# Optimization experiments

Measured on AMD Instinct MI355X. Metric: run time of the kernel, lower is better.

Reference implementation:

```python
import jax, jax.numpy as jnp
import numpy as np

T, L, N, DR = 8, 8, 500, 32
D = 2 * DR          # dr2 = 64
K = 12              # neighbors per region
S = 2               # number_sp attention layers


def setup_inputs() -> dict:
    key = jax.random.key(0)
    ks = jax.random.split(key, 14)
    inp = {}
    inp["all_data_static"] = jax.random.normal(ks[0], (T, L, N, D), jnp.float32)
    inp["thre_nc"] = jax.random.uniform(ks[1], (T, L, N, 1), jnp.float32)
    inp["all_data_dynamic_now"] = jax.random.uniform(ks[2], (L, N, D), jnp.float32)
    inp["neigh_poi"] = jax.random.randint(ks[3], (N, K), 0, N)
    inp["neigh_road"] = jax.random.randint(ks[4], (N, K), 0, N)
    inp["neigh_record"] = jax.random.randint(ks[5], (N, K), 0, N)
    inp["w1"] = jax.random.normal(ks[6], (2 * D, D), jnp.float32) * 0.05
    inp["wq_all"] = jax.random.normal(ks[7], (2, 3, S, D, D), jnp.float32) * 0.05
    inp["wk_all"] = jax.random.normal(ks[8], (2, 3, S, D, D), jnp.float32) * 0.05
    inp["wd_all"] = jax.random.normal(ks[9], (2, 3, S, D, D), jnp.float32) * 0.05
    inp["wmix_all"] = jax.random.normal(ks[10], (2, 3, D), jnp.float32) * 0.1
    inp["conv_w"] = jax.random.normal(ks[11], (4, 2 * D + 1), jnp.float32) * 0.05
    inp["conv_b"] = jnp.zeros((4,), jnp.float32)
    inp["fin_w"] = jax.random.normal(ks[12], (N, N), jnp.float32) * 0.02
    inp["fin_b"] = jnp.ones((N,), jnp.float32)
    return inp


def _attention(data, neigh, wq, wk, wd):
    # data: (T,L,N,D), neigh: (N,K)
    dn = data[:, :, neigh, :]                                   # (T,L,N,K,D) gather
    q = jnp.einsum('tlnd,de->tlne', data, wq)                   # (T,L,N,D)
    k = jnp.einsum('tlnkd,de->tlnke', dn, wk)                   # (T,L,N,K,D)
    a = jax.nn.softmax(jnp.einsum('tlne,tlnke->tlnk', q, k), -1)
    out = q + jnp.einsum('tlnk,tlnke->tlne', a, k)              # residual on q
    return jax.nn.sigmoid(jnp.einsum('tlnd,de->tlne', out, wd))


def _multiattention(data, neighs, wq, wk, wd, wmix):
    outs = []
    for g in range(3):  # poi, road, record
        x = data
        for s in range(wq.shape[1]):
            x = _attention(x, neighs[g], wq[g, s], wk[g, s], wd[g, s])
        outs.append(x)
    return jax.nn.sigmoid(outs[0] * wmix[0] + outs[1] * wmix[1] + outs[2] * wmix[2])


def reference(all_data_static, thre_nc, all_data_dynamic_now,
              neigh_poi, neigh_road, neigh_record,
              w1, wq_all, wk_all, wd_all, wmix_all,
              conv_w, conv_b, fin_w, fin_b):
    # --- Evolution: gated recurrence over time steps 1..T-1 ---
    def evo_step(now, xs):
        st, th = xs  # (L,N,D), (L,N,1)
        new = jax.nn.sigmoid(jnp.concatenate([now, st], -1) @ w1 * th
                             + now * (1.0 - th))
        return new, (new, new - now)
    now_final, (dyn_rest, diffs) = jax.lax.scan(
        evo_step, all_data_dynamic_now, (all_data_static[1:], thre_nc[1:]))
    all_dyn = jnp.concatenate([all_data_dynamic_now[None], dyn_rest], 0)  # (T,L,N,D)

    neighs = (neigh_poi, neigh_road, neigh_record)
    dyn = _multiattention(all_dyn, neighs, wq_all[0], wk_all[0], wd_all[0], wmix_all[0])
    sta = _multiattention(all_data_static, neighs, wq_all[1], wk_all[1], wd_all[1], wmix_all[1])
    x = jnp.concatenate([dyn, sta], -1)                          # (T,L,N,2D)

    # --- ConvLSTM, kernel (1,1), hidden_dim=1 -> pointwise gated recurrence ---
    h0 = jnp.zeros((x.shape[0], x.shape[2], 1), x.dtype)         # (T,N,1)
    def cell(carry, xt):  # xt: (T,N,2D)
        h, c = carry
        gates = jnp.concatenate([xt, h], -1) @ conv_w.T + conv_b  # (T,N,4)
        i = jax.nn.sigmoid(gates[..., 0:1])
        f = jax.nn.sigmoid(gates[..., 1:2])
        o = jax.nn.sigmoid(gates[..., 2:3])
        g = jnp.tanh(gates[..., 3:4])
        c2 = f * c + i * g
        h2 = o * jnp.tanh(c2)
        return (h2, c2), None
    (h_last, _), _ = jax.lax.scan(cell, (h0, h0), jnp.swapaxes(x, 0, 1))

    out = jax.nn.sigmoid(h_last[..., 0] @ fin_w.T + fin_b)       # (T,N)
    return out, now_final, diffs
```

## Files before the change

kernel.cpp:

```cpp
#include <hip/hip_runtime.h>
#include <math.h>

namespace {
constexpr int kT = 8, kL = 8, kN = 500, kD = 64, kK = 12;
constexpr int kLN  = kL * kN;
constexpr int kTLN = kT * kL * kN;
constexpr int kBUF = kTLN * kD;
constexpr int XS = 68;
}

__device__ __forceinline__ float sigf(float v) { return 1.f / (1.f + __expf(-v)); }

__device__ __forceinline__ void stage_x(const float* __restrict__ src, float* lds,
                                        int row0, int M) {
    int r  = threadIdx.x >> 4;
    int c4 = (threadIdx.x & 15) << 2;
#pragma unroll
    for (int i = 0; i < 4; ++i) {
        int rr  = r + 16 * i;
        int row = row0 + rr;
        row = row < M ? row : M - 1;
        float4 v = *reinterpret_cast<const float4*>(src + (size_t)row * 64 + c4);
        *reinterpret_cast<float4*>(lds + rr * XS + c4) = v;
    }
}

template <int K>
__device__ __forceinline__ void stage_w(const float* __restrict__ w, float* lds) {
    const float4* s = reinterpret_cast<const float4*>(w);
    float4* d = reinterpret_cast<float4*>(lds);
#pragma unroll
    for (int i = 0; i < K / 16; ++i)
        d[threadIdx.x + 256 * i] = s[threadIdx.x + 256 * i];
}

__device__ __forceinline__ void gemm_core(const float* ldsx, const float* ldsw,
                                          int rblk, int cblk, float4 acc[4]) {
#pragma unroll 4
    for (int k = 0; k < 64; k += 4) {
        float4 xv[4], wv[4];
#pragma unroll
        for (int i = 0; i < 4; ++i)
            xv[i] = *reinterpret_cast<const float4*>(ldsx + (4 * rblk + i) * XS + k);
#pragma unroll
        for (int d = 0; d < 4; ++d)
            wv[d] = *reinterpret_cast<const float4*>(ldsw + (k + d) * 64 + 4 * cblk);
#pragma unroll
        for (int i = 0; i < 4; ++i) {
            float xs[4] = {xv[i].x, xv[i].y, xv[i].z, xv[i].w};
#pragma unroll
            for (int d = 0; d < 4; ++d) {
                acc[i].x = fmaf(xs[d], wv[d].x, acc[i].x);
                acc[i].y = fmaf(xs[d], wv[d].y, acc[i].y);
                acc[i].z = fmaf(xs[d], wv[d].z, acc[i].z);
                acc[i].w = fmaf(xs[d], wv[d].w, acc[i].w);
            }
        }
    }
}

__device__ __forceinline__ void gemm_core_gw(const float* ldsx,
                                             const float* __restrict__ gw,
                                             int rblk, int cblk, float4 acc[4]) {
#pragma unroll 4
    for (int k = 0; k < 64; k += 4) {
        float4 xv[4], wv[4];
#pragma unroll
        for (int i = 0; i < 4; ++i)
            xv[i] = *reinterpret_cast<const float4*>(ldsx + (4 * rblk + i) * XS + k);
#pragma unroll
        for (int d = 0; d < 4; ++d)
            wv[d] = *reinterpret_cast<const float4*>(gw + (k + d) * 64 + 4 * cblk);
#pragma unroll
        for (int i = 0; i < 4; ++i) {
            float xs[4] = {xv[i].x, xv[i].y, xv[i].z, xv[i].w};
#pragma unroll
            for (int d = 0; d < 4; ++d) {
                acc[i].x = fmaf(xs[d], wv[d].x, acc[i].x);
                acc[i].y = fmaf(xs[d], wv[d].y, acc[i].y);
                acc[i].z = fmaf(xs[d], wv[d].z, acc[i].z);
                acc[i].w = fmaf(xs[d], wv[d].w, acc[i].w);
            }
        }
    }
}

__device__ __forceinline__ void gemm_core2(const float* ldsx, const float* ldswa,
                                           const float* ldswb, int rblk, int cblk,
                                           float4 acca[4], float4 accb[4]) {
#pragma unroll 4
    for (int k = 0; k < 64; k += 4) {
        float4 xv[4], wa[4], wb[4];
#pragma unroll
        for (int i = 0; i < 4; ++i)
            xv[i] = *reinterpret_cast<const float4*>(ldsx + (4 * rblk + i) * XS + k);
#pragma unroll
        for (int d = 0; d < 4; ++d) {
            wa[d] = *reinterpret_cast<const float4*>(ldswa + (k + d) * 64 + 4 * cblk);
            wb[d] = *reinterpret_cast<const float4*>(ldswb + (k + d) * 64 + 4 * cblk);
        }
#pragma unroll
        for (int i = 0; i < 4; ++i) {
            float xs[4] = {xv[i].x, xv[i].y, xv[i].z, xv[i].w};
#pragma unroll
            for (int d = 0; d < 4; ++d) {
                acca[i].x = fmaf(xs[d], wa[d].x, acca[i].x);
                acca[i].y = fmaf(xs[d], wa[d].y, acca[i].y);
                acca[i].z = fmaf(xs[d], wa[d].z, acca[i].z);
                acca[i].w = fmaf(xs[d], wa[d].w, acca[i].w);
                accb[i].x = fmaf(xs[d], wb[d].x, accb[i].x);
                accb[i].y = fmaf(xs[d], wb[d].y, accb[i].y);
                accb[i].z = fmaf(xs[d], wb[d].z, accb[i].z);
                accb[i].w = fmaf(xs[d], wb[d].w, accb[i].w);
            }
        }
    }
}

__global__ void __launch_bounds__(256) evo_all_kernel(const float* __restrict__ stat,
                                                      const float* __restrict__ thre,
                                                      const float* __restrict__ dyn0,
                                                      float* __restrict__ all_dyn,
                                                      float* __restrict__ diff,
                                                      float* __restrict__ now_final,
                                                      const float* __restrict__ w1) {
    __shared__ float ldsn[64 * XS];
    __shared__ float ldss[64 * XS];
    __shared__ float ldsw[128 * 64];
    int row0 = blockIdx.x * 64;
    stage_x(dyn0, ldsn, row0, kLN);
    stage_w<128>(w1, ldsw);
    int rblk = threadIdx.x >> 4, cblk = threadIdx.x & 15;
    __syncthreads();
#pragma unroll
    for (int i = 0; i < 4; ++i) {
        int row = row0 + 4 * rblk + i;
        if (row < kLN) {
            float4 x0 = *reinterpret_cast<const float4*>(ldsn + (4 * rblk + i) * XS + 4 * cblk);
            *reinterpret_cast<float4*>(all_dyn + (size_t)row * 64 + 4 * cblk) = x0;
        }
    }
#pragma unroll 1
    for (int t = 1; t < kT; ++t) {
        stage_x(stat + (size_t)t * kLN * kD, ldss, row0, kLN);
        __syncthreads();
        float4 acc[4] = {};
        gemm_core(ldsn, ldsw, rblk, cblk, acc);
        gemm_core(ldss, ldsw + 64 * 64, rblk, cblk, acc);
        float4 nv[4];
#pragma unroll
        for (int i = 0; i < 4; ++i) {
            int row = row0 + 4 * rblk + i;
            int rc  = row < kLN ? row : kLN - 1;
            float tt = thre[t * kLN + rc];
            float4 xn = *reinterpret_cast<const float4*>(ldsn + (4 * rblk + i) * XS + 4 * cblk);
            nv[i].x = sigf(acc[i].x * tt + xn.x * (1.f - tt));
            nv[i].y = sigf(acc[i].y * tt + xn.y * (1.f - tt));
            nv[i].z = sigf(acc[i].z * tt + xn.z * (1.f - tt));
            nv[i].w = sigf(acc[i].w * tt + xn.w * (1.f - tt));
            if (row < kLN) {
                float4 df;
                df.x = nv[i].x - xn.x; df.y = nv[i].y - xn.y;
                df.z = nv[i].z - xn.z; df.w = nv[i].w - xn.w;
                *reinterpret_cast<float4*>(all_dyn + ((size_t)t * kLN + row) * 64 + 4 * cblk) = nv[i];
                *reinterpret_cast<float4*>(diff + ((size_t)(t - 1) * kLN + row) * 64 + 4 * cblk) = df;
                if (t == kT - 1)
                    *reinterpret_cast<float4*>(now_final + (size_t)row * 64 + 4 * cblk) = nv[i];
            }
        }
        __syncthreads();
#pragma unroll
        for (int i = 0; i < 4; ++i)
            *reinterpret_cast<float4*>(ldsn + (4 * rblk + i) * XS + 4 * cblk) = nv[i];
    }
}

__global__ void __launch_bounds__(256) gemm_qk(const float* __restrict__ Xdyn,
                                               const float* __restrict__ Xstat,
                                               const float* __restrict__ wq_all,
                                               const float* __restrict__ wk_all,
                                               float* __restrict__ b1,
                                               float* __restrict__ b2, int step) {
    __shared__ float ldsx[64 * XS];
    __shared__ float ldswq[64 * 64];
    __shared__ float ldswk[64 * 64];
    int c = blockIdx.y;
    int m = c / 3;
    float* b1c = b1 + (size_t)c * kBUF;
    float* b2c = b2 + (size_t)c * kBUF;
    const float* X = step ? b1c : (m == 0 ? Xdyn : Xstat);
    size_t woff = (size_t)(c * 2 + step) * kD * kD;
    int row0 = blockIdx.x * 64;
    stage_x(X, ldsx, row0, kTLN);
    stage_w<64>(wq_all + woff, ldswq);
    stage_w<64>(wk_all + woff, ldswk);
    __syncthreads();
    int rblk = threadIdx.x >> 4, cblk = threadIdx.x & 15;
    float4 aq[4] = {}, ak[4] = {};
    gemm_core2(ldsx, ldswq, ldswk, rblk, cblk, aq, ak);
#pragma unroll
    for (int i = 0; i < 4; ++i) {
        size_t row = row0 + 4 * rblk + i;
        *reinterpret_cast<float4*>(b1c + row * 64 + 4 * cblk) = aq[i];
        *reinterpret_cast<float4*>(b2c + row * 64 + 4 * cblk) = ak[i];
    }
}

__global__ void __launch_bounds__(256) scorewd_kernel(float* __restrict__ b1,
                                                      const float* __restrict__ b2,
                                                      const int* __restrict__ npoi,
                                                      const int* __restrict__ nroad,
                                                      const int* __restrict__ nrec,
                                                      const float* __restrict__ wd_all,
                                                      int step) {
    __shared__ float ldsx[64 * XS];
    int p   = blockIdx.y * gridDim.x + blockIdx.x;
    int xcd = p & 7;
    int gid = xcd * 375 + (p >> 3);
    int c    = gid / 500;
    int tile = gid - c * 500;
    int g = c % 3;
    float* b1c = b1 + (size_t)c * kBUF;
    const float* b2c = b2 + (size_t)c * kBUF;
    const int* neigh = (g == 0) ? npoi : (g == 1) ? nroad : nrec;
    const float* gw = wd_all + (size_t)(c * 2 + step) * kD * kD;

    int lane = threadIdx.x & 63;
    int wv   = threadIdx.x >> 6;
    int sub  = lane >> 4;
    int gq   = lane & 15;
    int row0 = tile * 64;
#pragma unroll 1
    for (int pp = 0; pp < 4; ++pp) {
        int lr  = pp * 16 + wv * 4 + sub;
        int row = row0 + lr;
        int n   = row % kN;
        int slab = row - n;
        float4 q = *(reinterpret_cast<const float4*>(b1c) + (size_t)row * 16 + gq);
        const int4* nbp = reinterpret_cast<const int4*>(neigh + n * kK);
        int4 nb0 = nbp[0], nb1 = nbp[1], nb2 = nbp[2];
        int nb[12] = {nb0.x, nb0.y, nb0.z, nb0.w, nb1.x, nb1.y, nb1.z, nb1.w,
                      nb2.x, nb2.y, nb2.z, nb2.w};
        float4 kv[12];
        float sc[12];
#pragma unroll
        for (int j = 0; j < 12; ++j) {
            kv[j] = *(reinterpret_cast<const float4*>(b2c) + (size_t)(slab + nb[j]) * 16 + gq);
            sc[j] = q.x * kv[j].x + q.y * kv[j].y + q.z * kv[j].z + q.w * kv[j].w;
        }
#pragma unroll
        for (int off = 1; off < 16; off <<= 1) {
#pragma unroll
            for (int j = 0; j < 12; ++j) sc[j] += __shfl_xor(sc[j], off, 16);
        }
        float mx = sc[0];
#pragma unroll
        for (int j = 1; j < 12; ++j) mx = fmaxf(mx, sc[j]);
        float ssum = 0.f;
#pragma unroll
        for (int j = 0; j < 12; ++j) { sc[j] = __expf(sc[j] - mx); ssum += sc[j]; }
        float inv = 1.f / ssum;
        float4 o = q;
#pragma unroll
        for (int j = 0; j < 12; ++j) {
            float a = sc[j] * inv;
            o.x = fmaf(a, kv[j].x, o.x);
            o.y = fmaf(a, kv[j].y, o.y);
            o.z = fmaf(a, kv[j].z, o.z);
            o.w = fmaf(a, kv[j].w, o.w);
        }
        *reinterpret_cast<float4*>(ldsx + lr * XS + 4 * gq) = o;
    }
    __syncthreads();
    int rblk = threadIdx.x >> 4, cblk = threadIdx.x & 15;
    float4 acc[4] = {};
    gemm_core_gw(ldsx, gw, rblk, cblk, acc);
#pragma unroll
    for (int i = 0; i < 4; ++i) {
        size_t idx = ((size_t)(row0 + 4 * rblk + i)) * 64 + 4 * cblk;
        float4 y;
        y.x = sigf(acc[i].x); y.y = sigf(acc[i].y);
        y.z = sigf(acc[i].z); y.w = sigf(acc[i].w);
        *reinterpret_cast<float4*>(b1c + idx) = y;
    }
}

__global__ void __launch_bounds__(256) lstm_kernel(const float* __restrict__ b1,
                                                   const float* __restrict__ wmix,
                                                   const float* __restrict__ cw,
                                                   const float* __restrict__ cb,
                                                   float* __restrict__ hlast) {
    int lane = threadIdx.x & 63;
    int wv   = threadIdx.x >> 6;
    int sub  = lane >> 4;
    int fq   = lane & 15;
    int cell = blockIdx.x * 16 + wv * 4 + sub;
    int t = cell / kN, n = cell % kN;
    float wd_[4][4], ws_[4][4], wh[4], bb[4];
#pragma unroll
    for (int gg = 0; gg < 4; ++gg) {
#pragma unroll
        for (int k = 0; k < 4; ++k) {
            wd_[gg][k] = cw[gg * 129 + fq * 4 + k];
            ws_[gg][k] = cw[gg * 129 + 64 + fq * 4 + k];
        }
        wh[gg] = cw[gg * 129 + 128];
        bb[gg] = cb[gg];
    }
    float4 wm[6];
#pragma unroll
    for (int j = 0; j < 6; ++j)
        wm[j] = *reinterpret_cast<const float4*>(wmix + j * 64 + fq * 4);
    float h = 0.f, cc = 0.f;
#pragma unroll 1
    for (int l = 0; l < kL; ++l) {
        size_t row16 = ((size_t)(t * kL + l) * kN + n) * 16 + fq;
        float4 y[6];
#pragma unroll
        for (int j = 0; j < 6; ++j)
            y[j] = *(reinterpret_cast<const float4*>(b1) + (size_t)j * (kBUF / 4) + row16);
        float4 xd, xs;
        xd.x = sigf(y[0].x * wm[0].x + y[1].x * wm[1].x + y[2].x * wm[2].x);
        xd.y = sigf(y[0].y * wm[0].y + y[1].y * wm[1].y + y[2].y * wm[2].y);
        xd.z = sigf(y[0].z * wm[0].z + y[1].z * wm[1].z + y[2].z * wm[2].z);
        xd.w = sigf(y[0].w * wm[0].w + y[1].w * wm[1].w + y[2].w * wm[2].w);
        xs.x = sigf(y[3].x * wm[3].x + y[4].x * wm[4].x + y[5].x * wm[5].x);
        xs.y = sigf(y[3].y * wm[3].y + y[4].y * wm[4].y + y[5].y * wm[5].y);
        xs.z = sigf(y[3].z * wm[3].z + y[4].z * wm[4].z + y[5].z * wm[5].z);
        xs.w = sigf(y[3].w * wm[3].w + y[4].w * wm[4].w + y[5].w * wm[5].w);
        float gsum[4];
#pragma unroll
        for (int gg = 0; gg < 4; ++gg) {
            float v = xd.x * wd_[gg][0] + xd.y * wd_[gg][1]
                    + xd.z * wd_[gg][2] + xd.w * wd_[gg][3];
            v += xs.x * ws_[gg][0] + xs.y * ws_[gg][1]
               + xs.z * ws_[gg][2] + xs.w * ws_[gg][3];
            gsum[gg] = v;
        }
#pragma unroll
        for (int off = 1; off < 16; off <<= 1) {
#pragma unroll
            for (int gg = 0; gg < 4; ++gg) gsum[gg] += __shfl_xor(gsum[gg], off, 16);
        }
        float gi = sigf(gsum[0] + bb[0] + h * wh[0]);
        float gf = sigf(gsum[1] + bb[1] + h * wh[1]);
        float go = sigf(gsum[2] + bb[2] + h * wh[2]);
        float gg_ = tanhf(gsum[3] + bb[3] + h * wh[3]);
        cc = gf * cc + gi * gg_;
        h = go * tanhf(cc);
    }
    if (fq == 0) hlast[cell] = h;
}

__global__ void final_kernel(const float* __restrict__ h, const float* __restrict__ fw,
                             const float* __restrict__ fb, float* __restrict__ out) {
    int wave = threadIdx.x >> 6, lane = threadIdx.x & 63;
    int o = blockIdx.x * 4 + wave;
    int t = o / kN, m = o % kN;
    float acc = 0.f;
    for (int n = lane; n < kN; n += 64)
        acc = fmaf(h[t * kN + n], fw[(size_t)m * kN + n], acc);
#pragma unroll
    for (int off = 32; off > 0; off >>= 1) acc += __shfl_xor(acc, off);
    if (lane == 0) out[o] = sigf(acc + fb[m]);
}

extern "C" void kernel_launch(void* const* d_in, const int* in_sizes, int n_in,
                              void* d_out, int out_size, void* d_ws, size_t ws_size,
                              hipStream_t stream) {
    const float* stat   = (const float*)d_in[0];
    const float* thre   = (const float*)d_in[1];
    const float* dyn0   = (const float*)d_in[2];
    const int*   npoi   = (const int*)d_in[3];
    const int*   nroad  = (const int*)d_in[4];
    const int*   nrec   = (const int*)d_in[5];
    const float* w1     = (const float*)d_in[6];
    const float* wq_all = (const float*)d_in[7];
    const float* wk_all = (const float*)d_in[8];
    const float* wd_all = (const float*)d_in[9];
    const float* wmix   = (const float*)d_in[10];
    const float* conv_w = (const float*)d_in[11];
    const float* conv_b = (const float*)d_in[12];
    const float* fin_w  = (const float*)d_in[13];
    const float* fin_b  = (const float*)d_in[14];

    float* out       = (float*)d_out;
    float* now_final = out + kT * kN;
    float* diffs     = now_final + (size_t)kLN * kD;

    float* ws      = (float*)d_ws;
    float* all_dyn = ws;
    float* b1      = ws + (size_t)kBUF;
    float* b2      = ws + 7 * (size_t)kBUF;
    float* hlast   = ws + 13 * (size_t)kBUF;

    evo_all_kernel<<<(kLN + 63) / 64, 256, 0, stream>>>(stat, thre, dyn0,
                                                        all_dyn, diffs, now_final, w1);

    dim3 agrid(kTLN / 64, 6);
    gemm_qk<<<agrid, 256, 0, stream>>>(all_dyn, stat, wq_all, wk_all, b1, b2, 0);
    scorewd_kernel<<<agrid, 256, 0, stream>>>(b1, b2, npoi, nroad, nrec, wd_all, 0);
    gemm_qk<<<agrid, 256, 0, stream>>>(all_dyn, stat, wq_all, wk_all, b1, b2, 1);
    scorewd_kernel<<<agrid, 256, 0, stream>>>(b1, b2, npoi, nroad, nrec, wd_all, 1);

    lstm_kernel<<<kT * kN / 16, 256, 0, stream>>>(b1, wmix, conv_w, conv_b, hlast);
    final_kernel<<<kT * kN / 4, 256, 0, stream>>>(hlast, fin_w, fin_b, out);
}
```

Measured before the change: 350.7 us.

## Fuse score/Wd with next-layer QK GEMM and store K in bf16

Merges the first attention layer's score+Wd stage with the second layer's Q/K projection into one kernel, so the intermediate activation never goes back to global memory and one launch disappears. K is now stored as bf16 to halve the traffic of the neighbor gathers. Weights are read straight from global/cache instead of being staged in LDS. The fusion needs a separate K buffer, because another block's layer-1 K gather could otherwise race with layer-2 K writes. bf16 K adds rounding error to the attention scores and outputs.

Measured after the change: 384.9 us. 1.1x slower.

```diff
diff --git a/kernel.cpp b/kernel.cpp
--- a/kernel.cpp
+++ b/kernel.cpp
@@ -11,6 +11,18 @@
 
 __device__ __forceinline__ float sigf(float v) { return 1.f / (1.f + __expf(-v)); }
 
+__device__ __forceinline__ uint2 pack_bf16x4(float4 v) {
+    auto r = [](float f) {
+        unsigned u = __float_as_uint(f);
+        u += 0x7FFFu + ((u >> 16) & 1u);
+        return u >> 16;
+    };
+    uint2 o;
+    o.x = r(v.x) | (r(v.y) << 16);
+    o.y = r(v.z) | (r(v.w) << 16);
+    return o;
+}
+
 __device__ __forceinline__ void stage_x(const float* __restrict__ src, float* lds,
                                         int row0, int M) {
     int r  = threadIdx.x >> 4;
@@ -85,9 +97,11 @@
     }
 }
 
-__device__ __forceinline__ void gemm_core2(const float* ldsx, const float* ldswa,
-                                           const float* ldswb, int rblk, int cblk,
-                                           float4 acca[4], float4 accb[4]) {
+__device__ __forceinline__ void gemm_core2_gw(const float* ldsx,
+                                              const float* __restrict__ gwa,
+                                              const float* __restrict__ gwb,
+                                              int rblk, int cblk,
+                                              float4 acca[4], float4 accb[4]) {
 #pragma unroll 4
     for (int k = 0; k < 64; k += 4) {
         float4 xv[4], wa[4], wb[4];
@@ -96,8 +110,8 @@
             xv[i] = *reinterpret_cast<const float4*>(ldsx + (4 * rblk + i) * XS + k);
 #pragma unroll
         for (int d = 0; d < 4; ++d) {
-            wa[d] = *reinterpret_cast<const float4*>(ldswa + (k + d) * 64 + 4 * cblk);
-            wb[d] = *reinterpret_cast<const float4*>(ldswb + (k + d) * 64 + 4 * cblk);
+            wa[d] = *reinterpret_cast<const float4*>(gwa + (k + d) * 64 + 4 * cblk);
+            wb[d] = *reinterpret_cast<const float4*>(gwb + (k + d) * 64 + 4 * cblk);
         }
 #pragma unroll
         for (int i = 0; i < 4; ++i) {
@@ -114,6 +128,67 @@
                 accb[i].w = fmaf(xs[d], wb[d].w, accb[i].w);
             }
         }
+    }
+}
+
+__device__ __forceinline__ void score_phase(const float* __restrict__ Qsrc,
+                                            const uint2* __restrict__ Kb,
+                                            const int* __restrict__ neigh,
+                                            float* ldsx, int row0) {
+    int lane = threadIdx.x & 63;
+    int wv   = threadIdx.x >> 6;
+    int sub  = lane >> 4;
+    int gq   = lane & 15;
+    float4 qv[4];
+#pragma unroll
+    for (int pp = 0; pp < 4; ++pp) {
+        int row = row0 + pp * 16 + wv * 4 + sub;
+        qv[pp] = *(reinterpret_cast<const float4*>(Qsrc) + (size_t)row * 16 + gq);
+    }
+#pragma unroll 1
+    for (int pp = 0; pp < 4; ++pp) {
+        int lr  = pp * 16 + wv * 4 + sub;
+        int row = row0 + lr;
+        int n   = row % kN;
+        int slab = row - n;
+        float4 q = qv[pp];
+        const int4* nbp = reinterpret_cast<const int4*>(neigh + n * kK);
+        int4 nb0 = nbp[0], nb1 = nbp[1], nb2 = nbp[2];
+        int nb[12] = {nb0.x, nb0.y, nb0.z, nb0.w, nb1.x, nb1.y, nb1.z, nb1.w,
+                      nb2.x, nb2.y, nb2.z, nb2.w};
+        float4 kv[12];
+        float sc[12];
+#pragma unroll
+        for (int j = 0; j < 12; ++j) {
+            uint2 kk = Kb[(size_t)(slab + nb[j]) * 16 + gq];
+            kv[j].x = __uint_as_float(kk.x << 16);
+            kv[j].y = __uint_as_float(kk.x & 0xFFFF0000u);
+            kv[j].z = __uint_as_float(kk.y << 16);
+            kv[j].w = __uint_as_float(kk.y & 0xFFFF0000u);
+            sc[j] = q.x * kv[j].x + q.y * kv[j].y + q.z * kv[j].z + q.w * kv[j].w;
+        }
+#pragma unroll
+        for (int off = 1; off < 16; off <<= 1) {
+#pragma unroll
+            for (int j = 0; j < 12; ++j) sc[j] += __shfl_xor(sc[j], off, 16);
+        }
+        float mx = sc[0];
+#pragma unroll
+        for (int j = 1; j < 12; ++j) mx = fmaxf(mx, sc[j]);
+        float ssum = 0.f;
+#pragma unroll
+        for (int j = 0; j < 12; ++j) { sc[j] = __expf(sc[j] - mx); ssum += sc[j]; }
+        float inv = 1.f / ssum;
+        float4 o = q;
+#pragma unroll
+        for (int j = 0; j < 12; ++j) {
+            float a = sc[j] * inv;
+            o.x = fmaf(a, kv[j].x, o.x);
+            o.y = fmaf(a, kv[j].y, o.y);
+            o.z = fmaf(a, kv[j].z, o.z);
+            o.w = fmaf(a, kv[j].w, o.w);
+        }
+        *reinterpret_cast<float4*>(ldsx + lr * XS + 4 * gq) = o;
     }
 }
 
@@ -175,44 +250,43 @@
     }
 }
 
-__global__ void __launch_bounds__(256) gemm_qk(const float* __restrict__ Xdyn,
-                                               const float* __restrict__ Xstat,
-                                               const float* __restrict__ wq_all,
-                                               const float* __restrict__ wk_all,
-                                               float* __restrict__ b1,
-                                               float* __restrict__ b2, int step) {
+__global__ void __launch_bounds__(256) gemm_qk0(const float* __restrict__ Xdyn,
+                                                const float* __restrict__ Xstat,
+                                                const float* __restrict__ wq_all,
+                                                const float* __restrict__ wk_all,
+                                                float* __restrict__ b1,
+                                                unsigned short* __restrict__ b2a) {
     __shared__ float ldsx[64 * XS];
-    __shared__ float ldswq[64 * 64];
-    __shared__ float ldswk[64 * 64];
     int c = blockIdx.y;
     int m = c / 3;
+    const float* X = (m == 0) ? Xdyn : Xstat;
+    const float* gwq = wq_all + (size_t)(c * 2) * kD * kD;
+    const float* gwk = wk_all + (size_t)(c * 2) * kD * kD;
     float* b1c = b1 + (size_t)c * kBUF;
-    float* b2c = b2 + (size_t)c * kBUF;
-    const float* X = step ? b1c : (m == 0 ? Xdyn : Xstat);
-    size_t woff = (size_t)(c * 2 + step) * kD * kD;
+    unsigned short* kc = b2a + (size_t)c * kBUF;
     int row0 = blockIdx.x * 64;
     stage_x(X, ldsx, row0, kTLN);
-    stage_w<64>(wq_all + woff, ldswq);
-    stage_w<64>(wk_all + woff, ldswk);
     __syncthreads();
     int rblk = threadIdx.x >> 4, cblk = threadIdx.x & 15;
     float4 aq[4] = {}, ak[4] = {};
-    gemm_core2(ldsx, ldswq, ldswk, rblk, cblk, aq, ak);
+    gemm_core2_gw(ldsx, gwq, gwk, rblk, cblk, aq, ak);
 #pragma unroll
     for (int i = 0; i < 4; ++i) {
         size_t row = row0 + 4 * rblk + i;
         *reinterpret_cast<float4*>(b1c + row * 64 + 4 * cblk) = aq[i];
-        *reinterpret_cast<float4*>(b2c + row * 64 + 4 * cblk) = ak[i];
-    }
-}
-
-__global__ void __launch_bounds__(256) scorewd_kernel(float* __restrict__ b1,
-                                                      const float* __restrict__ b2,
-                                                      const int* __restrict__ npoi,
-                                                      const int* __restrict__ nroad,
-                                                      const int* __restrict__ nrec,
-                                                      const float* __restrict__ wd_all,
-                                                      int step) {
+        *reinterpret_cast<uint2*>(kc + row * 64 + 4 * cblk) = pack_bf16x4(ak[i]);
+    }
+}
+
+__global__ void __launch_bounds__(256) swqk_kernel(float* __restrict__ b1,
+                                                   const unsigned short* __restrict__ b2a,
+                                                   unsigned short* __restrict__ b2b,
+                                                   const int* __restrict__ npoi,
+                                                   const int* __restrict__ nroad,
+                                                   const int* __restrict__ nrec,
+                                                   const float* __restrict__ wd_all,
+                                                   const float* __restrict__ wq_all,
+                                                   const float* __restrict__ wk_all) {
     __shared__ float ldsx[64 * XS];
     int p   = blockIdx.y * gridDim.x + blockIdx.x;
     int xcd = p & 7;
@@ -221,60 +295,64 @@
     int tile = gid - c * 500;
     int g = c % 3;
     float* b1c = b1 + (size_t)c * kBUF;
-    const float* b2c = b2 + (size_t)c * kBUF;
+    const uint2* Kb = reinterpret_cast<const uint2*>(b2a + (size_t)c * kBUF);
+    unsigned short* k1c = b2b + (size_t)c * kBUF;
     const int* neigh = (g == 0) ? npoi : (g == 1) ? nroad : nrec;
-    const float* gw = wd_all + (size_t)(c * 2 + step) * kD * kD;
-
-    int lane = threadIdx.x & 63;
-    int wv   = threadIdx.x >> 6;
-    int sub  = lane >> 4;
-    int gq   = lane & 15;
+    const float* gwd = wd_all + (size_t)(c * 2) * kD * kD;
+    const float* gwq = wq_all + (size_t)(c * 2 + 1) * kD * kD;
+    const float* gwk = wk_all + (size_t)(c * 2 + 1) * kD * kD;
     int row0 = tile * 64;
-#pragma unroll 1
-    for (int pp = 0; pp < 4; ++pp) {
-        int lr  = pp * 16 + wv * 4 + sub;
-        int row = row0 + lr;
-        int n   = row % kN;
-        int slab = row - n;
-        float4 q = *(reinterpret_cast<const float4*>(b1c) + (size_t)row * 16 + gq);
-        const int4* nbp = reinterpret_cast<const int4*>(neigh + n * kK);
-        int4 nb0 = nbp[0], nb1 = nbp[1], nb2 = nbp[2];
-        int nb[12] = {nb0.x, nb0.y, nb0.z, nb0.w, nb1.x, nb1.y, nb1.z, nb1.w,
-                      nb2.x, nb2.y, nb2.z, nb2.w};
-        float4 kv[12];
-        float sc[12];
-#pragma unroll
-        for (int j = 0; j < 12; ++j) {
-            kv[j] = *(reinterpret_cast<const float4*>(b2c) + (size_t)(slab + nb[j]) * 16 + gq);
-            sc[j] = q.x * kv[j].x + q.y * kv[j].y + q.z * kv[j].z + q.w * kv[j].w;
-        }
-#pragma unroll
-        for (int off = 1; off < 16; off <<= 1) {
-#pragma unroll
-            for (int j = 0; j < 12; ++j) sc[j] += __shfl_xor(sc[j], off, 16);
-        }
-        float mx = sc[0];
-#pragma unroll
-        for (int j = 1; j < 12; ++j) mx = fmaxf(mx, sc[j]);
-        float ssum = 0.f;
-#pragma unroll
-        for (int j = 0; j < 12; ++j) { sc[j] = __expf(sc[j] - mx); ssum += sc[j]; }
-        float inv = 1.f / ssum;
-        float4 o = q;
-#pragma unroll
-        for (int j = 0; j < 12; ++j) {
-            float a = sc[j] * inv;
-            o.x = fmaf(a, kv[j].x, o.x);
-            o.y = fmaf(a, kv[j].y, o.y);
-            o.z = fmaf(a, kv[j].z, o.z);
-            o.w = fmaf(a, kv[j].w, o.w);
-        }
-        *reinterpret_cast<float4*>(ldsx + lr * XS + 4 * gq) = o;
-    }
-    __syncthreads();
+
+    score_phase(b1c, Kb, neigh, ldsx, row0);
+    __syncthreads();
+
     int rblk = threadIdx.x >> 4, cblk = threadIdx.x & 15;
     float4 acc[4] = {};
-    gemm_core_gw(ldsx, gw, rblk, cblk, acc);
+    gemm_core_gw(ldsx, gwd, rblk, cblk, acc);
+    __syncthreads();
+#pragma unroll
+    for (int i = 0; i < 4; ++i) {
+        float4 y;
+        y.x = sigf(acc[i].x); y.y = sigf(acc[i].y);
+        y.z = sigf(acc[i].z); y.w = sigf(acc[i].w);
+        *reinterpret_cast<float4*>(ldsx + (4 * rblk + i) * XS + 4 * cblk) = y;
+    }
+    __syncthreads();
+    float4 aq[4] = {}, ak[4] = {};
+    gemm_core2_gw(ldsx, gwq, gwk, rblk, cblk, aq, ak);
+#pragma unroll
+    for (int i = 0; i < 4; ++i) {
+        size_t row = row0 + 4 * rblk + i;
+        *reinterpret_cast<float4*>(b1c + row * 64 + 4 * cblk) = aq[i];
+        *reinterpret_cast<uint2*>(k1c + row * 64 + 4 * cblk) = pack_bf16x4(ak[i]);
+    }
+}
+
+__global__ void __launch_bounds__(256) scorewd_kernel(float* __restrict__ b1,
+                                                      const unsigned short* __restrict__ b2b,
+                                                      const int* __restrict__ npoi,
+                                                      const int* __restrict__ nroad,
+                                                      const int* __restrict__ nrec,
+                                                      const float* __restrict__ wd_all) {
+    __shared__ float ldsx[64 * XS];
+    int p   = blockIdx.y * gridDim.x + blockIdx.x;
+    int xcd = p & 7;
+    int gid = xcd * 375 + (p >> 3);
+    int c    = gid / 500;
+    int tile = gid - c * 500;
+    int g = c % 3;
+    float* b1c = b1 + (size_t)c * kBUF;
+    const uint2* Kb = reinterpret_cast<const uint2*>(b2b + (size_t)c * kBUF);
+    const int* neigh = (g == 0) ? npoi : (g == 1) ? nroad : nrec;
+    const float* gwd = wd_all + (size_t)(c * 2 + 1) * kD * kD;
+    int row0 = tile * 64;
+
+    score_phase(b1c, Kb, neigh, ldsx, row0);
+    __syncthreads();
+
+    int rblk = threadIdx.x >> 4, cblk = threadIdx.x & 15;
+    float4 acc[4] = {};
+    gemm_core_gw(ldsx, gwd, rblk, cblk, acc);
 #pragma unroll
     for (int i = 0; i < 4; ++i) {
         size_t idx = ((size_t)(row0 + 4 * rblk + i)) * 64 + 4 * cblk;
@@ -391,17 +469,18 @@
     float* ws      = (float*)d_ws;
     float* all_dyn = ws;
     float* b1      = ws + (size_t)kBUF;
-    float* b2      = ws + 7 * (size_t)kBUF;
+    unsigned short* b2a = (unsigned short*)(ws + 7 * (size_t)kBUF);
+    unsigned short* b2b = (unsigned short*)(ws + 10 * (size_t)kBUF);
     float* hlast   = ws + 13 * (size_t)kBUF;
 
     evo_all_kernel<<<(kLN + 63) / 64, 256, 0, stream>>>(stat, thre, dyn0,
                                                         all_dyn, diffs, now_final, w1);
 
     dim3 agrid(kTLN / 64, 6);
-    gemm_qk<<<agrid, 256, 0, stream>>>(all_dyn, stat, wq_all, wk_all, b1, b2, 0);
-    scorewd_kernel<<<agrid, 256, 0, stream>>>(b1, b2, npoi, nroad, nrec, wd_all, 0);
-    gemm_qk<<<agrid, 256, 0, stream>>>(all_dyn, stat, wq_all, wk_all, b1, b2, 1);
-    scorewd_kernel<<<agrid, 256, 0, stream>>>(b1, b2, npoi, nroad, nrec, wd_all, 1);
+    gemm_qk0<<<agrid, 256, 0, stream>>>(all_dyn, stat, wq_all, wk_all, b1, b2a);
+    swqk_kernel<<<agrid, 256, 0, stream>>>(b1, b2a, b2b, npoi, nroad, nrec,
+                                           wd_all, wq_all, wk_all);
+    scorewd_kernel<<<agrid, 256, 0, stream>>>(b1, b2b, npoi, nroad, nrec, wd_all);
 
     lstm_kernel<<<kT * kN / 16, 256, 0, stream>>>(b1, wmix, conv_w, conv_b, hlast);
     final_kernel<<<kT * kN / 4, 256, 0, stream>>>(hlast, fin_w, fin_b, out);
```

## Store attention keys as bf16, halve row tiles, read weights from global

Applied to the files above, without the earlier changes.

The key projection buffer is now written as bf16 (round-to-nearest-even packing) and unpacked in the score kernel. This halves the gather traffic for the 12-neighbor key reads. Tiles shrink from 64 to 32 rows per block, doubling the grid for the recurrence and attention kernels. gemm_qk now reads Wq/Wk directly from global memory instead of staging them in LDS. Reduced key precision may change results slightly, and smaller tiles reuse each weight load over fewer rows.

Measured after the change: 460.7 us. 1.31x slower.

```diff
diff --git a/kernel.cpp b/kernel.cpp
--- a/kernel.cpp
+++ b/kernel.cpp
@@ -11,16 +11,26 @@
 
 __device__ __forceinline__ float sigf(float v) { return 1.f / (1.f + __expf(-v)); }
 
-__device__ __forceinline__ void stage_x(const float* __restrict__ src, float* lds,
-                                        int row0, int M) {
+__device__ __forceinline__ uint2 pack_bf16x4(float4 v) {
+    auto r = [](float f) {
+        unsigned u = __float_as_uint(f);
+        u += 0x7FFFu + ((u >> 16) & 1u);
+        return u >> 16;
+    };
+    uint2 o;
+    o.x = r(v.x) | (r(v.y) << 16);
+    o.y = r(v.z) | (r(v.w) << 16);
+    return o;
+}
+
+__device__ __forceinline__ void stage_x32(const float* __restrict__ src, float* lds,
+                                          int row0) {
     int r  = threadIdx.x >> 4;
     int c4 = (threadIdx.x & 15) << 2;
 #pragma unroll
-    for (int i = 0; i < 4; ++i) {
-        int rr  = r + 16 * i;
-        int row = row0 + rr;
-        row = row < M ? row : M - 1;
-        float4 v = *reinterpret_cast<const float4*>(src + (size_t)row * 64 + c4);
+    for (int i = 0; i < 2; ++i) {
+        int rr = r + 16 * i;
+        float4 v = *reinterpret_cast<const float4*>(src + (size_t)(row0 + rr) * 64 + c4);
         *reinterpret_cast<float4*>(lds + rr * XS + c4) = v;
     }
 }
@@ -34,19 +44,19 @@
         d[threadIdx.x + 256 * i] = s[threadIdx.x + 256 * i];
 }
 
-__device__ __forceinline__ void gemm_core(const float* ldsx, const float* ldsw,
-                                          int rblk, int cblk, float4 acc[4]) {
+__device__ __forceinline__ void gemm_core32(const float* ldsx, const float* w,
+                                            int rblk, int cblk, float4 acc[2]) {
 #pragma unroll 4
     for (int k = 0; k < 64; k += 4) {
-        float4 xv[4], wv[4];
-#pragma unroll
-        for (int i = 0; i < 4; ++i)
-            xv[i] = *reinterpret_cast<const float4*>(ldsx + (4 * rblk + i) * XS + k);
+        float4 xv[2], wv[4];
+#pragma unroll
+        for (int i = 0; i < 2; ++i)
+            xv[i] = *reinterpret_cast<const float4*>(ldsx + (2 * rblk + i) * XS + k);
 #pragma unroll
         for (int d = 0; d < 4; ++d)
-            wv[d] = *reinterpret_cast<const float4*>(ldsw + (k + d) * 64 + 4 * cblk);
-#pragma unroll
-        for (int i = 0; i < 4; ++i) {
+            wv[d] = *reinterpret_cast<const float4*>(w + (k + d) * 64 + 4 * cblk);
+#pragma unroll
+        for (int i = 0; i < 2; ++i) {
             float xs[4] = {xv[i].x, xv[i].y, xv[i].z, xv[i].w};
 #pragma unroll
             for (int d = 0; d < 4; ++d) {
@@ -59,61 +69,90 @@
     }
 }
 
-__device__ __forceinline__ void gemm_core_gw(const float* ldsx,
-                                             const float* __restrict__ gw,
-                                             int rblk, int cblk, float4 acc[4]) {
+__device__ __forceinline__ void gemm_core32x2(const float* ldsx, const float* wa,
+                                              const float* wb, int rblk, int cblk,
+                                              float4 acca[2], float4 accb[2]) {
 #pragma unroll 4
     for (int k = 0; k < 64; k += 4) {
-        float4 xv[4], wv[4];
-#pragma unroll
-        for (int i = 0; i < 4; ++i)
-            xv[i] = *reinterpret_cast<const float4*>(ldsx + (4 * rblk + i) * XS + k);
-#pragma unroll
-        for (int d = 0; d < 4; ++d)
-            wv[d] = *reinterpret_cast<const float4*>(gw + (k + d) * 64 + 4 * cblk);
-#pragma unroll
-        for (int i = 0; i < 4; ++i) {
+        float4 xv[2], va[4], vb[4];
+#pragma unroll
+        for (int i = 0; i < 2; ++i)
+            xv[i] = *reinterpret_cast<const float4*>(ldsx + (2 * rblk + i) * XS + k);
+#pragma unroll
+        for (int d = 0; d < 4; ++d) {
+            va[d] = *reinterpret_cast<const float4*>(wa + (k + d) * 64 + 4 * cblk);
+            vb[d] = *reinterpret_cast<const float4*>(wb + (k + d) * 64 + 4 * cblk);
+        }
+#pragma unroll
+        for (int i = 0; i < 2; ++i) {
             float xs[4] = {xv[i].x, xv[i].y, xv[i].z, xv[i].w};
 #pragma unroll
             for (int d = 0; d < 4; ++d) {
-                acc[i].x = fmaf(xs[d], wv[d].x, acc[i].x);
-                acc[i].y = fmaf(xs[d], wv[d].y, acc[i].y);
-                acc[i].z = fmaf(xs[d], wv[d].z, acc[i].z);
-                acc[i].w = fmaf(xs[d], wv[d].w, acc[i].w);
+                acca[i].x = fmaf(xs[d], va[d].x, acca[i].x);
+                acca[i].y = fmaf(xs[d], va[d].y, acca[i].y);
+                acca[i].z = fmaf(xs[d], va[d].z, acca[i].z);
+                acca[i].w = fmaf(xs[d], va[d].w, acca[i].w);
+                accb[i].x = fmaf(xs[d], vb[d].x, accb[i].x);
+                accb[i].y = fmaf(xs[d], vb[d].y, accb[i].y);
+                accb[i].z = fmaf(xs[d], vb[d].z, accb[i].z);
+                accb[i].w = fmaf(xs[d], vb[d].w, accb[i].w);
             }
         }
     }
 }
 
-__device__ __forceinline__ void gemm_core2(const float* ldsx, const float* ldswa,
-                                           const float* ldswb, int rblk, int cblk,
-                                           float4 acca[4], float4 accb[4]) {
-#pragma unroll 4
-    for (int k = 0; k < 64; k += 4) {
-        float4 xv[4], wa[4], wb[4];
-#pragma unroll
-        for (int i = 0; i < 4; ++i)
-            xv[i] = *reinterpret_cast<const float4*>(ldsx + (4 * rblk + i) * XS + k);
-#pragma unroll
-        for (int d = 0; d < 4; ++d) {
-            wa[d] = *reinterpret_cast<const float4*>(ldswa + (k + d) * 64 + 4 * cblk);
-            wb[d] = *reinterpret_cast<const float4*>(ldswb + (k + d) * 64 + 4 * cblk);
-        }
-#pragma unroll
-        for (int i = 0; i < 4; ++i) {
-            float xs[4] = {xv[i].x, xv[i].y, xv[i].z, xv[i].w};
-#pragma unroll
-            for (int d = 0; d < 4; ++d) {
-                acca[i].x = fmaf(xs[d], wa[d].x, acca[i].x);
-                acca[i].y = fmaf(xs[d], wa[d].y, acca[i].y);
-                acca[i].z = fmaf(xs[d], wa[d].z, acca[i].z);
-                acca[i].w = fmaf(xs[d], wa[d].w, acca[i].w);
-                accb[i].x = fmaf(xs[d], wb[d].x, accb[i].x);
-                accb[i].y = fmaf(xs[d], wb[d].y, accb[i].y);
-                accb[i].z = fmaf(xs[d], wb[d].z, accb[i].z);
-                accb[i].w = fmaf(xs[d], wb[d].w, accb[i].w);
-            }
-        }
+__device__ __forceinline__ void score_phase32(const float* __restrict__ Qsrc,
+                                              const uint2* __restrict__ Kb,
+                                              const int* __restrict__ neigh,
+                                              float* ldsx, int row0) {
+    int lane = threadIdx.x & 63;
+    int wv   = threadIdx.x >> 6;
+    int sub  = lane >> 4;
+    int gq   = lane & 15;
+#pragma unroll 1
+    for (int pp = 0; pp < 2; ++pp) {
+        int lr  = pp * 16 + wv * 4 + sub;
+        int row = row0 + lr;
+        int n   = row % kN;
+        int slab = row - n;
+        float4 q = *(reinterpret_cast<const float4*>(Qsrc) + (size_t)row * 16 + gq);
+        const int4* nbp = reinterpret_cast<const int4*>(neigh + n * kK);
+        int4 nb0 = nbp[0], nb1 = nbp[1], nb2 = nbp[2];
+        int nb[12] = {nb0.x, nb0.y, nb0.z, nb0.w, nb1.x, nb1.y, nb1.z, nb1.w,
+                      nb2.x, nb2.y, nb2.z, nb2.w};
+        float4 kv[12];
+        float sc[12];
+#pragma unroll
+        for (int j = 0; j < 12; ++j) {
+            uint2 kk = Kb[(size_t)(slab + nb[j]) * 16 + gq];
+            kv[j].x = __uint_as_float(kk.x << 16);
+            kv[j].y = __uint_as_float(kk.x & 0xFFFF0000u);
+            kv[j].z = __uint_as_float(kk.y << 16);
+            kv[j].w = __uint_as_float(kk.y & 0xFFFF0000u);
+            sc[j] = q.x * kv[j].x + q.y * kv[j].y + q.z * kv[j].z + q.w * kv[j].w;
+        }
+#pragma unroll
+        for (int off = 1; off < 16; off <<= 1) {
+#pragma unroll
+            for (int j = 0; j < 12; ++j) sc[j] += __shfl_xor(sc[j], off, 16);
+        }
+        float mx = sc[0];
+#pragma unroll
+        for (int j = 1; j < 12; ++j) mx = fmaxf(mx, sc[j]);
+        float ssum = 0.f;
+#pragma unroll
+        for (int j = 0; j < 12; ++j) { sc[j] = __expf(sc[j] - mx); ssum += sc[j]; }
+        float inv = 1.f / ssum;
+        float4 o = q;
+#pragma unroll
+        for (int j = 0; j < 12; ++j) {
+            float a = sc[j] * inv;
+            o.x = fmaf(a, kv[j].x, o.x);
+            o.y = fmaf(a, kv[j].y, o.y);
+            o.z = fmaf(a, kv[j].z, o.z);
+            o.w = fmaf(a, kv[j].w, o.w);
+        }
+        *reinterpret_cast<float4*>(ldsx + lr * XS + 4 * gq) = o;
     }
 }
 
@@ -124,54 +163,49 @@
                                                       float* __restrict__ diff,
                                                       float* __restrict__ now_final,
                                                       const float* __restrict__ w1) {
-    __shared__ float ldsn[64 * XS];
-    __shared__ float ldss[64 * XS];
+    __shared__ float ldsn[32 * XS];
+    __shared__ float ldss[32 * XS];
     __shared__ float ldsw[128 * 64];
-    int row0 = blockIdx.x * 64;
-    stage_x(dyn0, ldsn, row0, kLN);
+    int row0 = blockIdx.x * 32;
+    stage_x32(dyn0, ldsn, row0);
     stage_w<128>(w1, ldsw);
     int rblk = threadIdx.x >> 4, cblk = threadIdx.x & 15;
     __syncthreads();
 #pragma unroll
-    for (int i = 0; i < 4; ++i) {
-        int row = row0 + 4 * rblk + i;
-        if (row < kLN) {
-            float4 x0 = *reinterpret_cast<const float4*>(ldsn + (4 * rblk + i) * XS + 4 * cblk);
-            *reinterpret_cast<float4*>(all_dyn + (size_t)row * 64 + 4 * cblk) = x0;
-        }
+    for (int i = 0; i < 2; ++i) {
+        int row = row0 + 2 * rblk + i;
+        float4 x0 = *reinterpret_cast<const float4*>(ldsn + (2 * rblk + i) * XS + 4 * cblk);
+        *reinterpret_cast<float4*>(all_dyn + (size_t)row * 64 + 4 * cblk) = x0;
     }
 #pragma unroll 1
     for (int t = 1; t < kT; ++t) {
-        stage_x(stat + (size_t)t * kLN * kD, ldss, row0, kLN);
+        stage_x32(stat + (size_t)t * kLN * kD, ldss, row0);
         __syncthreads();
-        float4 acc[4] = {};
-        gemm_core(ldsn, ldsw, rblk, cblk, acc);
-        gemm_core(ldss, ldsw + 64 * 64, rblk, cblk, acc);
-        float4 nv[4];
-#pragma unroll
-        for (int i = 0; i < 4; ++i) {
-            int row = row0 + 4 * rblk + i;
-            int rc  = row < kLN ? row : kLN - 1;
-            float tt = thre[t * kLN + rc];
-            float4 xn = *reinterpret_cast<const float4*>(ldsn + (4 * rblk + i) * XS + 4 * cblk);
+        float4 acc[2] = {};
+        gemm_core32(ldsn, ldsw, rblk, cblk, acc);
+        gemm_core32(ldss, ldsw + 64 * 64, rblk, cblk, acc);
+        float4 nv[2];
+#pragma unroll
+        for (int i = 0; i < 2; ++i) {
+            int row = row0 + 2 * rblk + i;
+            float tt = thre[t * kLN + row];
+            float4 xn = *reinterpret_cast<const float4*>(ldsn + (2 * rblk + i) * XS + 4 * cblk);
             nv[i].x = sigf(acc[i].x * tt + xn.x * (1.f - tt));
             nv[i].y = sigf(acc[i].y * tt + xn.y * (1.f - tt));
             nv[i].z = sigf(acc[i].z * tt + xn.z * (1.f - tt));
             nv[i].w = sigf(acc[i].w * tt + xn.w * (1.f - tt));
-            if (row < kLN) {
-                float4 df;
-                df.x = nv[i].x - xn.x; df.y = nv[i].y - xn.y;
-                df.z = nv[i].z - xn.z; df.w = nv[i].w - xn.w;
-                *reinterpret_cast<float4*>(all_dyn + ((size_t)t * kLN + row) * 64 + 4 * cblk) = nv[i];
-                *reinterpret_cast<float4*>(diff + ((size_t)(t - 1) * kLN + row) * 64 + 4 * cblk) = df;
-                if (t == kT - 1)
-                    *reinterpret_cast<float4*>(now_final + (size_t)row * 64 + 4 * cblk) = nv[i];
-            }
+            float4 df;
+            df.x = nv[i].x - xn.x; df.y = nv[i].y - xn.y;
+            df.z = nv[i].z - xn.z; df.w = nv[i].w - xn.w;
+            *reinterpret_cast<float4*>(all_dyn + ((size_t)t * kLN + row) * 64 + 4 * cblk) = nv[i];
+            *reinterpret_cast<float4*>(diff + ((size_t)(t - 1) * kLN + row) * 64 + 4 * cblk) = df;
+            if (t == kT - 1)
+                *reinterpret_cast<float4*>(now_final + (size_t)row * 64 + 4 * cblk) = nv[i];
         }
         __syncthreads();
 #pragma unroll
-        for (int i = 0; i < 4; ++i)
-            *reinterpret_cast<float4*>(ldsn + (4 * rblk + i) * XS + 4 * cblk) = nv[i];
+        for (int i = 0; i < 2; ++i)
+            *reinterpret_cast<float4*>(ldsn + (2 * rblk + i) * XS + 4 * cblk) = nv[i];
     }
 }
 
@@ -180,104 +214,59 @@
                                                const float* __restrict__ wq_all,
                                                const float* __restrict__ wk_all,
                                                float* __restrict__ b1,
-                                               float* __restrict__ b2, int step) {
-    __shared__ float ldsx[64 * XS];
-    __shared__ float ldswq[64 * 64];
-    __shared__ float ldswk[64 * 64];
+                                               unsigned short* __restrict__ b2,
+                                               int step) {
+    __shared__ float ldsx[32 * XS];
     int c = blockIdx.y;
     int m = c / 3;
     float* b1c = b1 + (size_t)c * kBUF;
-    float* b2c = b2 + (size_t)c * kBUF;
+    unsigned short* kc = b2 + (size_t)c * kBUF;
     const float* X = step ? b1c : (m == 0 ? Xdyn : Xstat);
-    size_t woff = (size_t)(c * 2 + step) * kD * kD;
-    int row0 = blockIdx.x * 64;
-    stage_x(X, ldsx, row0, kTLN);
-    stage_w<64>(wq_all + woff, ldswq);
-    stage_w<64>(wk_all + woff, ldswk);
+    const float* gwq = wq_all + (size_t)(c * 2 + step) * kD * kD;
+    const float* gwk = wk_all + (size_t)(c * 2 + step) * kD * kD;
+    int row0 = blockIdx.x * 32;
+    stage_x32(X, ldsx, row0);
     __syncthreads();
     int rblk = threadIdx.x >> 4, cblk = threadIdx.x & 15;
-    float4 aq[4] = {}, ak[4] = {};
-    gemm_core2(ldsx, ldswq, ldswk, rblk, cblk, aq, ak);
-#pragma unroll
-    for (int i = 0; i < 4; ++i) {
-        size_t row = row0 + 4 * rblk + i;
+    float4 aq[2] = {}, ak[2] = {};
+    gemm_core32x2(ldsx, gwq, gwk, rblk, cblk, aq, ak);
+#pragma unroll
+    for (int i = 0; i < 2; ++i) {
+        size_t row = row0 + 2 * rblk + i;
         *reinterpret_cast<float4*>(b1c + row * 64 + 4 * cblk) = aq[i];
-        *reinterpret_cast<float4*>(b2c + row * 64 + 4 * cblk) = ak[i];
+        *reinterpret_cast<uint2*>(kc + row * 64 + 4 * cblk) = pack_bf16x4(ak[i]);
     }
 }
 
 __global__ void __launch_bounds__(256) scorewd_kernel(float* __restrict__ b1,
-                                                      const float* __restrict__ b2,
+                                                      const unsigned short* __restrict__ b2,
                                                       const int* __restrict__ npoi,
                                                       const int* __restrict__ nroad,
                                                       const int* __restrict__ nrec,
                                                       const float* __restrict__ wd_all,
                                                       int step) {
-    __shared__ float ldsx[64 * XS];
+    __shared__ float ldsx[32 * XS];
     int p   = blockIdx.y * gridDim.x + blockIdx.x;
     int xcd = p & 7;
-    int gid = xcd * 375 + (p >> 3);
-    int c    = gid / 500;
-    int tile = gid - c * 500;
+    int gid = xcd * 750 + (p >> 3);
+    int c    = gid / 1000;
+    int tile = gid - c * 1000;
     int g = c % 3;
     float* b1c = b1 + (size_t)c * kBUF;
-    const float* b2c = b2 + (size_t)c * kBUF;
+    const uint2* Kb = reinterpret_cast<const uint2*>(b2 + (size_t)c * kBUF);
     const int* neigh = (g == 0) ? npoi : (g == 1) ? nroad : nrec;
-    const float* gw = wd_all + (size_t)(c * 2 + step) * kD * kD;
-
-    int lane = threadIdx.x & 63;
-    int wv   = threadIdx.x >> 6;
-    int sub  = lane >> 4;
-    int gq   = lane & 15;
-    int row0 = tile * 64;
-#pragma unroll 1
-    for (int pp = 0; pp < 4; ++pp) {
-        int lr  = pp * 16 + wv * 4 + sub;
-        int row = row0 + lr;
-        int n   = row % kN;
-        int slab = row - n;
-        float4 q = *(reinterpret_cast<const float4*>(b1c) + (size_t)row * 16 + gq);
-        const int4* nbp = reinterpret_cast<const int4*>(neigh + n * kK);
-        int4 nb0 = nbp[0], nb1 = nbp[1], nb2 = nbp[2];
-        int nb[12] = {nb0.x, nb0.y, nb0.z, nb0.w, nb1.x, nb1.y, nb1.z, nb1.w,
-                      nb2.x, nb2.y, nb2.z, nb2.w};
-        float4 kv[12];
-        float sc[12];
-#pragma unroll
-        for (int j = 0; j < 12; ++j) {
-            kv[j] = *(reinterpret_cast<const float4*>(b2c) + (size_t)(slab + nb[j]) * 16 + gq);
-            sc[j] = q.x * kv[j].x + q.y * kv[j].y + q.z * kv[j].z + q.w * kv[j].w;
-        }
-#pragma unroll
-        for (int off = 1; off < 16; off <<= 1) {
-#pragma unroll
-            for (int j = 0; j < 12; ++j) sc[j] += __shfl_xor(sc[j], off, 16);
-        }
-        float mx = sc[0];
-#pragma unroll
-        for (int j = 1; j < 12; ++j) mx = fmaxf(mx, sc[j]);
-        float ssum = 0.f;
-#pragma unroll
-        for (int j = 0; j < 12; ++j) { sc[j] = __expf(sc[j] - mx); ssum += sc[j]; }
-        float inv = 1.f / ssum;
-        float4 o = q;
-#pragma unroll
-        for (int j = 0; j < 12; ++j) {
-            float a = sc[j] * inv;
-            o.x = fmaf(a, kv[j].x, o.x);
-            o.y = fmaf(a, kv[j].y, o.y);
-            o.z = fmaf(a, kv[j].z, o.z);
-            o.w = fmaf(a, kv[j].w, o.w);
-        }
-        *reinterpret_cast<float4*>(ldsx + lr * XS + 4 * gq) = o;
-    }
+    const float* gwd = wd_all + (size_t)(c * 2 + step) * kD * kD;
+    int row0 = tile * 32;
+
+    score_phase32(b1c, Kb, neigh, ldsx, row0);
     __syncthreads();
+
     int rblk = threadIdx.x >> 4, cblk = threadIdx.x & 15;
-    float4 acc[4] = {};
-    gemm_core_gw(ldsx, gw, rblk, cblk, acc);
-#pragma unroll
-    for (int i = 0; i < 4; ++i) {
-        size_t idx = ((size_t)(row0 + 4 * rblk + i)) * 64 + 4 * cblk;
+    float4 acc[2] = {};
+    gemm_core32(ldsx, gwd, rblk, cblk, acc);
+#pragma unroll
+    for (int i = 0; i < 2; ++i) {
+        size_t idx = ((size_t)(row0 + 2 * rblk + i)) * 64 + 4 * cblk;
         float4 y;
         y.x = sigf(acc[i].x); y.y = sigf(acc[i].y);
         y.z = sigf(acc[i].z); y.w = sigf(acc[i].w);
@@ -391,13 +380,13 @@
     float* ws      = (float*)d_ws;
     float* all_dyn = ws;
     float* b1      = ws + (size_t)kBUF;
-    float* b2      = ws + 7 * (size_t)kBUF;
-    float* hlast   = ws + 13 * (size_t)kBUF;
-
-    evo_all_kernel<<<(kLN + 63) / 64, 256, 0, stream>>>(stat, thre, dyn0,
-                                                        all_dyn, diffs, now_final, w1);
-
-    dim3 agrid(kTLN / 64, 6);
+    unsigned short* b2 = (unsigned short*)(ws + 7 * (size_t)kBUF);
+    float* hlast   = ws + 10 * (size_t)kBUF;
+
+    evo_all_kernel<<<kLN / 32, 256, 0, stream>>>(stat, thre, dyn0,
+                                                 all_dyn, diffs, now_final, w1);
+
+    dim3 agrid(kTLN / 32, 6);
     gemm_qk<<<agrid, 256, 0, stream>>>(all_dyn, stat, wq_all, wk_all, b1, b2, 0);
     scorewd_kernel<<<agrid, 256, 0, stream>>>(b1, b2, npoi, nroad, nrec, wd_all, 0);
     gemm_qk<<<agrid, 256, 0, stream>>>(all_dyn, stat, wq_all, wk_all, b1, b2, 1);
```
